# Kernel tuning notes

Hardware: AMD Instinct MI355X
Metric: run time of the kernel (lower is better)

The kernel has to match this reference:

```python
import jax, jax.numpy as jnp
import numpy as np

NB_KNN = (10, 20, 100, 200)   # values of k to evaluate; max_k = 200
T = 0.07                       # softmax temperature
NUM_CLASSES = 1000


def setup_inputs() -> dict:
    key = jax.random.key(0)
    k1, k2, k3 = jax.random.split(key, 3)
    features_rank = jax.random.normal(k1, (256, 512), jnp.float32)      # (B, d) query features
    train_features = jax.random.normal(k2, (100000, 512), jnp.float32)  # (N, d) train bank
    train_labels = jax.random.randint(k3, (100000,), 0, NUM_CLASSES)     # (N,) int labels
    return {"features_rank": features_rank, "train_features": train_features,
            "train_labels": train_labels}


def _knn_probs(features_rank, train_features, train_labels):
    max_k = max(NB_KNN)
    # similarity: (B, N) = (B, d) @ (d, N)  -- mirrors torch.mm(broadcasted, train_features_rank_T)
    sims = features_rank @ train_features.T
    topk_sims, idx = jax.lax.top_k(sims, max_k)          # (B, max_k), sorted descending
    neighbors = train_labels[idx]                         # (B, max_k) gathered labels
    w = jax.nn.softmax(topk_sims / T, axis=1)             # (B, max_k) neighbor weights
    B = features_rank.shape[0]
    rows = jnp.arange(B)[:, None]                         # (B, 1) row indices for scatter
    # Instead of materializing one_hot (B, max_k, C) and summing prefixes,
    # scatter-add the first k weights into per-class buckets (same math, fused).
    probs = [jnp.zeros((B, NUM_CLASSES), w.dtype).at[rows, neighbors[:, :k]].add(w[:, :k])
             for k in NB_KNN]
    return jnp.stack(probs, axis=0)                       # (len(NB_KNN), B, C)


def reference(features_rank, train_features, train_labels):
    return _knn_probs(features_rank, train_features, train_labels)
```

## Files before the change

kernel.cpp:

```cpp
#include <hip/hip_runtime.h>
#include <math.h>

#define KDIM   512
#define NCLS   1000
#define CUTOFF 3.0f
#define MAXCAP 4096
#define BN     64
#define BK     64
#define NSTAGE (KDIM / BK)
#define FCAP   512

typedef __attribute__((ext_vector_type(8))) short  short8;
typedef __attribute__((ext_vector_type(4))) float  floatx4;

__device__ __forceinline__ unsigned enc_f(float f) {
    unsigned u = __float_as_uint(f);
    return (u & 0x80000000u) ? ~u : (u | 0x80000000u);
}
__device__ __forceinline__ float dec_f(unsigned k) {
    unsigned u = (k & 0x80000000u) ? (k & 0x7FFFFFFFu) : ~k;
    return __uint_as_float(u);
}
__device__ __forceinline__ unsigned short f2bf(float f) {
    unsigned u = __float_as_uint(f);
    u += 0x7FFFu + ((u >> 16) & 1u);
    return (unsigned short)(u >> 16);
}
__device__ __forceinline__ float bf2f(unsigned short h) {
    return __uint_as_float(((unsigned)h) << 16);
}

__device__ __forceinline__ void gload_lds16(const float* g, float* l) {
    __builtin_amdgcn_global_load_lds(
        (const __attribute__((address_space(1))) void*)g,
        (__attribute__((address_space(3))) void*)l, 16, 0, 0);
}

__global__ void k_prep(const float* __restrict__ A, unsigned short* __restrict__ af,
                       unsigned* __restrict__ cnt, unsigned* __restrict__ gmax, int Brows) {
    int t = blockIdx.x * blockDim.x + threadIdx.x;
    if (t < Brows) { cnt[t] = 0u; gmax[t] = enc_f(-3.0e38f); }
    if (t >= Brows * (KDIM / 8)) return;
    int r = t >> 6;
    int o = t & 63;
    int s16 = r >> 4, c = o >> 2, kq = o & 3;
    int lane = kq * 16 + (r & 15);
    const float* src = A + (size_t)r * KDIM + o * 8;
    size_t bhi = ((size_t)((s16 * 16 + c) * 2 + 0) * 64 + lane) * 8;
    size_t blo = ((size_t)((s16 * 16 + c) * 2 + 1) * 64 + lane) * 8;
#pragma unroll
    for (int j = 0; j < 8; ++j) {
        float f = src[j];
        unsigned short h = f2bf(f);
        af[bhi + j] = h;
        af[blo + j] = f2bf(f - bf2f(h));
    }
}

__global__ __launch_bounds__(512, 4) void k_gemm(
    const float* __restrict__ Bt,
    const unsigned short* __restrict__ af,
    float* __restrict__ cand_val, int* __restrict__ cand_idx,
    unsigned* __restrict__ cnt, unsigned* __restrict__ gmax,
    int N, int cap)
{
    __shared__ float Bs[2][4096];

    const int tid  = threadIdx.x;
    const int lane = tid & 63;
    const int wid  = tid >> 6;
    const int colBase = blockIdx.x * BN;

    const float* srcg[2];
    unsigned     dst_f[2];
#pragma unroll
    for (int i = 0; i < 2; ++i) {
        const int bs  = wid * 2048 + i * 1024 + lane * 16;
        const int b   = bs ^ (((bs >> 8) & 7) << 4);
        const int col = b >> 8;
        const int k0  = (b & 255) >> 2;
        int gcol = colBase + col;
        if (gcol >= N) gcol = 0;
        srcg[i]  = Bt + (size_t)gcol * KDIM + k0;
        dst_f[i] = (unsigned)((wid * 2048 + i * 1024) >> 2);
    }

    const int rb = (((lane & 15) * 256) + ((lane >> 4) * 32)) ^ ((lane & 7) << 4);

    floatx4 acc[2][4];
#pragma unroll
    for (int rt = 0; rt < 2; ++rt)
#pragma unroll
        for (int ct = 0; ct < 4; ++ct)
            acc[rt][ct] = (floatx4){0.f, 0.f, 0.f, 0.f};

#pragma unroll
    for (int i = 0; i < 2; ++i)
        gload_lds16(srcg[i], &Bs[0][dst_f[i]]);
    __syncthreads();

    for (int s = 0; s < NSTAGE; ++s) {
        short8 aH[2][2], aL[2][2];
#pragma unroll
        for (int chunk = 0; chunk < 2; ++chunk) {
            const int cg = s * 2 + chunk;
#pragma unroll
            for (int rt = 0; rt < 2; ++rt) {
                const int s16 = wid * 2 + rt;
                size_t sl = (size_t)((s16 * 16 + cg) * 2) * 64 + lane;
                aH[chunk][rt] = *(const short8*)(af + sl * 8);
                aL[chunk][rt] = *(const short8*)(af + (sl + 64) * 8);
            }
        }

        if (s + 1 < NSTAGE) {
#pragma unroll
            for (int i = 0; i < 2; ++i)
                gload_lds16(srcg[i] + (size_t)(s + 1) * BK, &Bs[(s + 1) & 1][dst_f[i]]);
        }

        __builtin_amdgcn_s_setprio(1);
#pragma unroll
        for (int chunk = 0; chunk < 2; ++chunk) {
#pragma unroll
            for (int ct = 0; ct < 4; ++ct) {
                const int fb = (rb + ct * 4096 + chunk * 128) >> 2;
                float4 p0 = *(const float4*)&Bs[s & 1][fb];
                float4 p1 = *(const float4*)&Bs[s & 1][fb ^ 4];
                union { float4 v[2]; float f[8]; } P;
                union { short8 v; unsigned short u[8]; } H, L;
                P.v[0] = p0; P.v[1] = p1;
#pragma unroll
                for (int j = 0; j < 8; ++j) {
                    unsigned short h = f2bf(P.f[j]);
                    H.u[j] = h; L.u[j] = f2bf(P.f[j] - bf2f(h));
                }
#pragma unroll
                for (int rt = 0; rt < 2; ++rt) {
                    acc[rt][ct] = __builtin_amdgcn_mfma_f32_16x16x32_bf16(aH[chunk][rt], H.v, acc[rt][ct], 0, 0, 0);
                    acc[rt][ct] = __builtin_amdgcn_mfma_f32_16x16x32_bf16(aH[chunk][rt], L.v, acc[rt][ct], 0, 0, 0);
                    acc[rt][ct] = __builtin_amdgcn_mfma_f32_16x16x32_bf16(aL[chunk][rt], H.v, acc[rt][ct], 0, 0, 0);
                }
            }
        }
        __builtin_amdgcn_s_setprio(0);
        __syncthreads();
    }

    const int q   = lane >> 4;
    const int n15 = lane & 15;
#pragma unroll
    for (int rt = 0; rt < 2; ++rt) {
#pragma unroll
        for (int reg = 0; reg < 4; ++reg) {
            const int row = wid * 32 + rt * 16 + q * 4 + reg;
            float m = fmaxf(fmaxf(acc[rt][0][reg], acc[rt][1][reg]),
                            fmaxf(acc[rt][2][reg], acc[rt][3][reg]));
#pragma unroll
            for (int off = 1; off < 16; off <<= 1) m = fmaxf(m, __shfl_xor(m, off));
            unsigned oldk = 0u;
            if (n15 == 0) oldk = atomicMax(&gmax[row], enc_f(m));
            oldk = (unsigned)__shfl((int)oldk, lane & 48);
            const float thr = fmaxf(dec_f(oldk), m) - CUTOFF;
#pragma unroll
            for (int ct = 0; ct < 4; ++ct) {
                const float v = acc[rt][ct][reg];
                const int col = colBase + ct * 16 + n15;
                if (v >= thr && col < N) {
                    unsigned p = atomicAdd(&cnt[row], 1u);
                    if (p < (unsigned)cap) {
                        cand_val[(size_t)row * cap + p] = v;
                        cand_idx[(size_t)row * cap + p] = col;
                    }
                }
            }
        }
    }
}

__global__ __launch_bounds__(256) void k_finalize(
    const float* __restrict__ cand_val,
    const int* __restrict__ cand_idx,
    const unsigned* __restrict__ cnt,
    const unsigned* __restrict__ gmax,
    const int* __restrict__ labels,
    float* __restrict__ out,
    int Brows, int cap)
{
    __shared__ float s_val[FCAP];
    __shared__ int   s_idx[FCAP];
    __shared__ float s_out[4 * NCLS];
    __shared__ int   s_n;
    __shared__ float s_part[4];
    __shared__ float s_Z;

    const int row = blockIdx.x;
    const int tid = threadIdx.x;
    if (tid == 0) s_n = 0;
    __syncthreads();

    const float m   = dec_f(gmax[row]);
    const float thr = m - CUTOFF;
    const int n = min((int)cnt[row], cap);
    for (int i = tid; i < n; i += 256) {
        float v = cand_val[(size_t)row * cap + i];
        if (v >= thr) {
            int p = atomicAdd(&s_n, 1);
            if (p < FCAP) { s_val[p] = v; s_idx[p] = cand_idx[(size_t)row * cap + i]; }
        }
    }
    for (int c = tid; c < 4 * NCLS; c += 256) s_out[c] = 0.f;
    __syncthreads();
    const int ns = min(s_n, FCAP);

    float e0 = 0.f, e1 = 0.f;
    int   r0 = 0x7fffffff, r1 = 0x7fffffff;
    int   lab0 = 0, lab1 = 0;
    if (tid < ns) {
        const float v = s_val[tid]; const int ix = s_idx[tid];
        int rk = 0;
        for (int j = 0; j < ns; ++j) {
            const float vj = s_val[j];
            rk += (vj > v || (vj == v && s_idx[j] < ix)) ? 1 : 0;
        }
        r0 = rk;
        if (rk < 200) { e0 = expf((v - m) * (1.0f / 0.07f)); lab0 = labels[ix]; }
    }
    if (tid + 256 < ns) {
        const int i2 = tid + 256;
        const float v = s_val[i2]; const int ix = s_idx[i2];
        int rk = 0;
        for (int j = 0; j < ns; ++j) {
            const float vj = s_val[j];
            rk += (vj > v || (vj == v && s_idx[j] < ix)) ? 1 : 0;
        }
        r1 = rk;
        if (rk < 200) { e1 = expf((v - m) * (1.0f / 0.07f)); lab1 = labels[ix]; }
    }

    float part = e0 + e1;
#pragma unroll
    for (int off = 32; off >= 1; off >>= 1) part += __shfl_down(part, off);
    if ((tid & 63) == 0) s_part[tid >> 6] = part;
    __syncthreads();
    if (tid == 0) s_Z = (s_part[0] + s_part[1]) + (s_part[2] + s_part[3]);
    __syncthreads();
    const float invZ = 1.0f / s_Z;

    if (r0 < 200) {
        const float w = e0 * invZ;
        if (r0 < 10)  atomicAdd(&s_out[0 * NCLS + lab0], w);
        if (r0 < 20)  atomicAdd(&s_out[1 * NCLS + lab0], w);
        if (r0 < 100) atomicAdd(&s_out[2 * NCLS + lab0], w);
        atomicAdd(&s_out[3 * NCLS + lab0], w);
    }
    if (r1 < 200) {
        const float w = e1 * invZ;
        if (r1 < 10)  atomicAdd(&s_out[0 * NCLS + lab1], w);
        if (r1 < 20)  atomicAdd(&s_out[1 * NCLS + lab1], w);
        if (r1 < 100) atomicAdd(&s_out[2 * NCLS + lab1], w);
        atomicAdd(&s_out[3 * NCLS + lab1], w);
    }
    __syncthreads();

    for (int c = tid; c < 4 * NCLS; c += 256) {
        const int sl = c / NCLS, cc = c - sl * NCLS;
        out[(size_t)sl * ((size_t)Brows * NCLS) + (size_t)row * NCLS + cc] = s_out[c];
    }
}

extern "C" void kernel_launch(void* const* d_in, const int* in_sizes, int n_in,
                              void* d_out, int out_size, void* d_ws, size_t ws_size,
                              hipStream_t stream) {
    const float* A      = (const float*)d_in[0];
    const float* Bt     = (const float*)d_in[1];
    const int*   labels = (const int*)d_in[2];
    float* out = (float*)d_out;

    const int Brows = in_sizes[0] / KDIM;
    const int N     = in_sizes[2];

    size_t af_elems = (size_t)Brows * KDIM * 2;
    unsigned short* af = (unsigned short*)d_ws;
    unsigned* cnt  = (unsigned*)(af + af_elems);
    unsigned* gmax = cnt + Brows;
    char* rest = (char*)(gmax + Brows);
    size_t used  = (size_t)(rest - (char*)d_ws);
    size_t avail = (ws_size > used) ? (ws_size - used) : 0;
    int cap = (int)((avail / ((size_t)Brows * 8)) < (size_t)MAXCAP
                        ? (avail / ((size_t)Brows * 8)) : (size_t)MAXCAP);
    if (cap < 1) cap = 1;
    float* cand_val = (float*)rest;
    int*   cand_idx = (int*)(cand_val + (size_t)Brows * cap);

    k_prep<<<(Brows * (KDIM / 8) + 255) / 256, 256, 0, stream>>>(A, af, cnt, gmax, Brows);
    k_gemm<<<(N + BN - 1) / BN, 512, 0, stream>>>(Bt, af, cand_val, cand_idx, cnt, gmax, N, cap);
    k_finalize<<<Brows, 256, 0, stream>>>(cand_val, cand_idx, cnt, gmax, labels, out, Brows, cap);
}
```

Baseline: 400.9 us.

## Load B tiles directly from global to registers and drop LDS staging

Removes the LDS double buffer and the global_load_lds staging with its per-stage barriers. Each lane now reads its B fragment straight from global memory into registers, using software double-buffered register prefetch across the 16 k-chunks. The bf16 hi/lo split now uses packed v_cvt_pk_bf16_f32 conversions, and the occupancy hint of 4 blocks is dropped from launch bounds. In exchange, B data is no longer shared across the 8 waves through LDS, so each wave reloads the same columns from global or L2, and register pressure rises.

Measured after the change: 537.3 us. +34.0%, slower.

```diff
diff --git a/kernel.cpp b/kernel.cpp
--- a/kernel.cpp
+++ b/kernel.cpp
@@ -6,8 +6,6 @@
 #define CUTOFF 3.0f
 #define MAXCAP 4096
 #define BN     64
-#define BK     64
-#define NSTAGE (KDIM / BK)
 #define FCAP   512
 
 typedef __attribute__((ext_vector_type(8))) short  short8;
@@ -29,11 +27,10 @@
 __device__ __forceinline__ float bf2f(unsigned short h) {
     return __uint_as_float(((unsigned)h) << 16);
 }
-
-__device__ __forceinline__ void gload_lds16(const float* g, float* l) {
-    __builtin_amdgcn_global_load_lds(
-        (const __attribute__((address_space(1))) void*)g,
-        (__attribute__((address_space(3))) void*)l, 16, 0, 0);
+__device__ __forceinline__ unsigned cvtpk(float a, float b) {
+    unsigned r;
+    asm("v_cvt_pk_bf16_f32 %0, %1, %2" : "=v"(r) : "v"(a), "v"(b));
+    return r;
 }
 
 __global__ void k_prep(const float* __restrict__ A, unsigned short* __restrict__ af,
@@ -57,35 +54,27 @@
     }
 }
 
-__global__ __launch_bounds__(512, 4) void k_gemm(
+__global__ __launch_bounds__(512) void k_gemm(
     const float* __restrict__ Bt,
     const unsigned short* __restrict__ af,
     float* __restrict__ cand_val, int* __restrict__ cand_idx,
     unsigned* __restrict__ cnt, unsigned* __restrict__ gmax,
     int N, int cap)
 {
-    __shared__ float Bs[2][4096];
-
     const int tid  = threadIdx.x;
     const int lane = tid & 63;
     const int wid  = tid >> 6;
     const int colBase = blockIdx.x * BN;
 
-    const float* srcg[2];
-    unsigned     dst_f[2];
-#pragma unroll
-    for (int i = 0; i < 2; ++i) {
-        const int bs  = wid * 2048 + i * 1024 + lane * 16;
-        const int b   = bs ^ (((bs >> 8) & 7) << 4);
-        const int col = b >> 8;
-        const int k0  = (b & 255) >> 2;
-        int gcol = colBase + col;
-        if (gcol >= N) gcol = 0;
-        srcg[i]  = Bt + (size_t)gcol * KDIM + k0;
-        dst_f[i] = (unsigned)((wid * 2048 + i * 1024) >> 2);
-    }
-
-    const int rb = (((lane & 15) * 256) + ((lane >> 4) * 32)) ^ ((lane & 7) << 4);
+    const int c15 = lane & 15;
+    const int kq  = lane >> 4;
+    const float* bbase[4];
+#pragma unroll
+    for (int ct = 0; ct < 4; ++ct) {
+        int col = colBase + ct * 16 + c15;
+        if (col >= N) col = 0;
+        bbase[ct] = Bt + (size_t)col * KDIM + kq * 8;
+    }
 
     floatx4 acc[2][4];
 #pragma unroll
@@ -94,58 +83,71 @@
         for (int ct = 0; ct < 4; ++ct)
             acc[rt][ct] = (floatx4){0.f, 0.f, 0.f, 0.f};
 
-#pragma unroll
-    for (int i = 0; i < 2; ++i)
-        gload_lds16(srcg[i], &Bs[0][dst_f[i]]);
-    __syncthreads();
-
-    for (int s = 0; s < NSTAGE; ++s) {
-        short8 aH[2][2], aL[2][2];
-#pragma unroll
-        for (int chunk = 0; chunk < 2; ++chunk) {
-            const int cg = s * 2 + chunk;
-#pragma unroll
-            for (int rt = 0; rt < 2; ++rt) {
-                const int s16 = wid * 2 + rt;
-                size_t sl = (size_t)((s16 * 16 + cg) * 2) * 64 + lane;
-                aH[chunk][rt] = *(const short8*)(af + sl * 8);
-                aL[chunk][rt] = *(const short8*)(af + (sl + 64) * 8);
-            }
-        }
-
-        if (s + 1 < NSTAGE) {
-#pragma unroll
-            for (int i = 0; i < 2; ++i)
-                gload_lds16(srcg[i] + (size_t)(s + 1) * BK, &Bs[(s + 1) & 1][dst_f[i]]);
-        }
-
-        __builtin_amdgcn_s_setprio(1);
-#pragma unroll
-        for (int chunk = 0; chunk < 2; ++chunk) {
-#pragma unroll
-            for (int ct = 0; ct < 4; ++ct) {
-                const int fb = (rb + ct * 4096 + chunk * 128) >> 2;
-                float4 p0 = *(const float4*)&Bs[s & 1][fb];
-                float4 p1 = *(const float4*)&Bs[s & 1][fb ^ 4];
-                union { float4 v[2]; float f[8]; } P;
-                union { short8 v; unsigned short u[8]; } H, L;
-                P.v[0] = p0; P.v[1] = p1;
-#pragma unroll
-                for (int j = 0; j < 8; ++j) {
-                    unsigned short h = f2bf(P.f[j]);
-                    H.u[j] = h; L.u[j] = f2bf(P.f[j] - bf2f(h));
-                }
-#pragma unroll
-                for (int rt = 0; rt < 2; ++rt) {
-                    acc[rt][ct] = __builtin_amdgcn_mfma_f32_16x16x32_bf16(aH[chunk][rt], H.v, acc[rt][ct], 0, 0, 0);
-                    acc[rt][ct] = __builtin_amdgcn_mfma_f32_16x16x32_bf16(aH[chunk][rt], L.v, acc[rt][ct], 0, 0, 0);
-                    acc[rt][ct] = __builtin_amdgcn_mfma_f32_16x16x32_bf16(aL[chunk][rt], H.v, acc[rt][ct], 0, 0, 0);
-                }
-            }
-        }
-        __builtin_amdgcn_s_setprio(0);
-        __syncthreads();
-    }
+#define LOAD_A(AH, AL, CG) do {                                            \
+    _Pragma("unroll")                                                      \
+    for (int rt = 0; rt < 2; ++rt) {                                       \
+        const int s16 = wid * 2 + rt;                                      \
+        size_t sl = (size_t)(((s16 * 16 + (CG)) * 2)) * 64 + lane;         \
+        (AH)[rt] = *(const short8*)(af + sl * 8);                          \
+        (AL)[rt] = *(const short8*)(af + (sl + 64) * 8);                   \
+    } } while (0)
+
+#define LOAD_B(BA, BB, CG) do {                                            \
+    _Pragma("unroll")                                                      \
+    for (int ct = 0; ct < 4; ++ct) {                                       \
+        const float* p = bbase[ct] + (CG) * 32;                            \
+        (BA)[ct] = *(const float4*)(p);                                    \
+        (BB)[ct] = *(const float4*)(p + 4);                                \
+    } } while (0)
+
+#define COMPUTE(BA, BB, AH, AL) do {                                       \
+    _Pragma("unroll")                                                      \
+    for (int ct = 0; ct < 4; ++ct) {                                       \
+        union { unsigned w[4]; short8 v; } H, L;                           \
+        float f0 = (BA)[ct].x, f1 = (BA)[ct].y,                            \
+              f2 = (BA)[ct].z, f3 = (BA)[ct].w;                            \
+        float f4 = (BB)[ct].x, f5 = (BB)[ct].y,                            \
+              f6 = (BB)[ct].z, f7 = (BB)[ct].w;                            \
+        H.w[0] = cvtpk(f0, f1); H.w[1] = cvtpk(f2, f3);                    \
+        H.w[2] = cvtpk(f4, f5); H.w[3] = cvtpk(f6, f7);                    \
+        float h0 = __uint_as_float(H.w[0] << 16);                          \
+        float h1 = __uint_as_float(H.w[0] & 0xFFFF0000u);                  \
+        float h2 = __uint_as_float(H.w[1] << 16);                          \
+        float h3 = __uint_as_float(H.w[1] & 0xFFFF0000u);                  \
+        float h4 = __uint_as_float(H.w[2] << 16);                          \
+        float h5 = __uint_as_float(H.w[2] & 0xFFFF0000u);                  \
+        float h6 = __uint_as_float(H.w[3] << 16);                          \
+        float h7 = __uint_as_float(H.w[3] & 0xFFFF0000u);                  \
+        L.w[0] = cvtpk(f0 - h0, f1 - h1);                                  \
+        L.w[1] = cvtpk(f2 - h2, f3 - h3);                                  \
+        L.w[2] = cvtpk(f4 - h4, f5 - h5);                                  \
+        L.w[3] = cvtpk(f6 - h6, f7 - h7);                                  \
+        _Pragma("unroll")                                                  \
+        for (int rt = 0; rt < 2; ++rt) {                                   \
+            acc[rt][ct] = __builtin_amdgcn_mfma_f32_16x16x32_bf16((AH)[rt], H.v, acc[rt][ct], 0, 0, 0); \
+            acc[rt][ct] = __builtin_amdgcn_mfma_f32_16x16x32_bf16((AH)[rt], L.v, acc[rt][ct], 0, 0, 0); \
+            acc[rt][ct] = __builtin_amdgcn_mfma_f32_16x16x32_bf16((AL)[rt], H.v, acc[rt][ct], 0, 0, 0); \
+        } } } while (0)
+
+    float4 ba[4], bb[4], na[4], nb[4];
+    short8 aH[2], aL[2], nH[2], nL[2];
+    LOAD_B(ba, bb, 0);
+    LOAD_A(aH, aL, 0);
+
+#pragma unroll
+    for (int cg = 0; cg < 16; cg += 2) {
+        LOAD_B(na, nb, cg + 1);
+        LOAD_A(nH, nL, cg + 1);
+        COMPUTE(ba, bb, aH, aL);
+        if (cg + 2 < 16) {
+            LOAD_B(ba, bb, cg + 2);
+            LOAD_A(aH, aL, cg + 2);
+        }
+        COMPUTE(na, nb, nH, nL);
+    }
+#undef LOAD_A
+#undef LOAD_B
+#undef COMPUTE
 
     const int q   = lane >> 4;
     const int n15 = lane & 15;
```
